# Optimization experiments

Measured on AMD Instinct MI355X. Metric: run time of the kernel, lower is better.

## Reference

```python
import jax, jax.numpy as jnp
import numpy as np
import math

N, T, C = 2, 2048, 2048   # batch, seq, dim_in
H, DQK, DV = 16, 128, 128  # heads, dim_qk, dim_v


def setup_inputs() -> dict:
    key = jax.random.key(0)
    ks = jax.random.split(key, 5)
    x = jax.random.normal(ks[0], (N, T, C), dtype=jnp.float32)
    # randw(*d) = randn(*d) / sqrt(d[-1]); last dim is dim_in=C for all weights
    scale = 1.0 / math.sqrt(C)
    w_q = jax.random.normal(ks[1], (H, DQK, C), dtype=jnp.float32) * scale
    w_k = jax.random.normal(ks[2], (H, DQK, C), dtype=jnp.float32) * scale
    w_v = jax.random.normal(ks[3], (H, DV, C), dtype=jnp.float32) * scale
    # original w_o is [DV*H, C]; stored here as its intended [H, DV, C] view
    w_o = jax.random.normal(ks[4], (H, DV, C), dtype=jnp.float32) * scale
    return {"x": x, "w_q": w_q, "w_k": w_k, "w_v": w_v, "w_o": w_o}


def reference(x, w_q, w_k, w_v, w_o):
    # QKV projections: [N,T,C] x [H,D,C] -> [N,H,T,D]
    q = jnp.einsum('ntc,hdc->nhtd', x, w_q)
    k = jnp.einsum('ntc,hdc->nhtd', x, w_k)
    v = jnp.einsum('ntc,hdc->nhtd', x, w_v)
    # attention scores [N,H,T,S]
    a = jnp.einsum('nhtd,nhsd->nhts', q, k) / math.sqrt(DQK)
    t = x.shape[1]
    causal_mask = jnp.tril(jnp.ones((t, t), dtype=bool))  # [T,S]
    a = jnp.where(causal_mask[None, None, :, :], a, -jnp.inf)
    a = jax.nn.softmax(a, axis=3)
    # dropout=0.0 -> no-op
    y = jnp.einsum('nhts,nhsd->nthd', a, v)  # [N,T,H,DV]
    out = jnp.einsum('nthd,hdc->ntc', y, w_o)
    return (out, k, v)
```

## Files before the change

### kernel.cpp

```cpp
#include <hip/hip_runtime.h>
#include <math.h>

#define NB 2
#define TT 2048
#define CC 2048
#define HH 16
#define DD 128

#define ELEMS_OUT ((size_t)NB * TT * CC)
#define ELEMS_KV  ((size_t)NB * HH * TT * DD)

typedef __attribute__((ext_vector_type(8))) short bf16x8;
typedef __attribute__((ext_vector_type(4))) float f32x4;

__device__ __forceinline__ void split_bf16(float v, unsigned short& hi, unsigned short& lo) {
    const unsigned u = __float_as_uint(v);
    hi = (unsigned short)(u >> 16);
    const float r = v - __uint_as_float(u & 0xffff0000u);
    lo = (unsigned short)(__float_as_uint(r) >> 16);
}

__device__ __forceinline__ unsigned short bf16_rtn(float v) {
    unsigned u = __float_as_uint(v);
    u += 0x7fff + ((u >> 16) & 1);
    return (unsigned short)(u >> 16);
}

__global__ __launch_bounds__(256)
void conv_hl(const float* __restrict__ src, unsigned short* __restrict__ hi,
             unsigned short* __restrict__ lo, int n4)
{
    for (int i = blockIdx.x * 256 + threadIdx.x; i < n4; i += gridDim.x * 256) {
        const float4 v = ((const float4*)src)[i];
        unsigned short h0, h1, h2, h3, l0, l1, l2, l3;
        split_bf16(v.x, h0, l0);
        split_bf16(v.y, h1, l1);
        split_bf16(v.z, h2, l2);
        split_bf16(v.w, h3, l3);
        ((ushort4*)hi)[i] = make_ushort4(h0, h1, h2, h3);
        ((ushort4*)lo)[i] = make_ushort4(l0, l1, l2, l3);
    }
}

__global__ __launch_bounds__(256)
void tconv_kernel(const float* __restrict__ src, unsigned short* __restrict__ dhi,
                  unsigned short* __restrict__ dlo)
{
    __shared__ float T[32][33];
    const int tx = threadIdx.x & 31;
    const int ty = threadIdx.x >> 5;
    const int c0 = blockIdx.x * 32;
    const int r0 = blockIdx.y * 32;
#pragma unroll
    for (int i = 0; i < 4; ++i)
        T[ty + 8 * i][tx] = src[(size_t)(r0 + ty + 8 * i) * 2048 + c0 + tx];
    __syncthreads();
#pragma unroll
    for (int i = 0; i < 4; ++i) {
        const float v = T[tx][ty + 8 * i];
        unsigned short h, l;
        split_bf16(v, h, l);
        const size_t o = (size_t)(c0 + ty + 8 * i) * 2048 + r0 + tx;
        dhi[o] = h;
        dlo[o] = l;
    }
}

#define MFMA_GEMM_BODY(AHI, ALO, BHI, BLO, M0, J0)                                   \
    const int tid  = threadIdx.x;                                                    \
    const int lane = tid & 63;                                                       \
    const int w    = tid >> 6;                                                       \
    const int wr   = w >> 1, wc = w & 1;                                             \
    const int lr   = lane & 15, g = lane >> 4;                                       \
    __shared__ __align__(16) unsigned short As[2][4][129][8];                        \
    __shared__ __align__(16) unsigned short Bs[2][4][129][8];                        \
    f32x4 acc[4][4];                                                                 \
    _Pragma("unroll")                                                                \
    for (int m = 0; m < 4; ++m)                                                      \
        _Pragma("unroll")                                                            \
        for (int n = 0; n < 4; ++n) acc[m][n] = (f32x4){0.f, 0.f, 0.f, 0.f};         \
    for (int kt = 0; kt < CC; kt += 32) {                                            \
        __syncthreads();                                                             \
        _Pragma("unroll")                                                            \
        for (int it = 0; it < 4; ++it) {                                             \
            const int hl   = it >> 1;                                                \
            const int rem  = tid + (it & 1) * 256;                                   \
            const int row  = rem >> 2;                                               \
            const int slot = rem & 3;                                                \
            const unsigned short* ap = (hl ? ALO : AHI)                              \
                + (size_t)(M0 + row) * 2048 + kt + slot * 8;                         \
            *(bf16x8*)&As[hl][slot][row][0] = *(const bf16x8*)ap;                    \
            const unsigned short* bp = (hl ? BLO : BHI)                              \
                + (size_t)(J0 + row) * 2048 + kt + slot * 8;                         \
            *(bf16x8*)&Bs[hl][slot][row][0] = *(const bf16x8*)bp;                    \
        }                                                                            \
        __syncthreads();                                                             \
        bf16x8 ah[4], al[4];                                                         \
        _Pragma("unroll")                                                            \
        for (int m = 0; m < 4; ++m) {                                                \
            ah[m] = *(const bf16x8*)&As[0][g][wr * 64 + m * 16 + lr][0];             \
            al[m] = *(const bf16x8*)&As[1][g][wr * 64 + m * 16 + lr][0];             \
        }                                                                            \
        _Pragma("unroll")                                                            \
        for (int n = 0; n < 4; ++n) {                                                \
            const bf16x8 bh = *(const bf16x8*)&Bs[0][g][wc * 64 + n * 16 + lr][0];   \
            const bf16x8 bl = *(const bf16x8*)&Bs[1][g][wc * 64 + n * 16 + lr][0];   \
            _Pragma("unroll")                                                        \
            for (int m = 0; m < 4; ++m) {                                            \
                f32x4 t = acc[m][n];                                                 \
                t = __builtin_amdgcn_mfma_f32_16x16x32_bf16(al[m], bh, t, 0, 0, 0);  \
                t = __builtin_amdgcn_mfma_f32_16x16x32_bf16(ah[m], bl, t, 0, 0, 0);  \
                t = __builtin_amdgcn_mfma_f32_16x16x32_bf16(ah[m], bh, t, 0, 0, 0);  \
                acc[m][n] = t;                                                       \
            }                                                                        \
        }                                                                            \
    }

__global__ __launch_bounds__(256, 3)
void mfma_qkv_kernel(const unsigned short* __restrict__ ahi,
                     const unsigned short* __restrict__ alo,
                     const unsigned short* __restrict__ bhi,
                     const unsigned short* __restrict__ blo,
                     float* __restrict__ qb, float* __restrict__ kb,
                     float* __restrict__ vb)
{
    const int j0 = blockIdx.x * 128;
    const int m0 = blockIdx.y * 128;
    MFMA_GEMM_BODY(ahi, alo, bhi, blo, m0, j0)

    const int p = j0 >> 11;
    const int h = (j0 & 2047) >> 7;
    float* outb = (p == 0) ? qb : ((p == 1) ? kb : vb);
#pragma unroll
    for (int m = 0; m < 4; ++m) {
#pragma unroll
        for (int r = 0; r < 4; ++r) {
            const int gm = m0 + wr * 64 + m * 16 + g * 4 + r;
            const int nb = gm >> 11;
            const int t  = gm & 2047;
            float* rowp = outb + ((size_t)(nb * HH + h) * TT + t) * DD;
#pragma unroll
            for (int n = 0; n < 4; ++n)
                rowp[wc * 64 + n * 16 + lr] = acc[m][n][r];
        }
    }
}

__global__ __launch_bounds__(256, 3)
void mfma_oproj_kernel(const unsigned short* __restrict__ ahi,
                       const unsigned short* __restrict__ alo,
                       const unsigned short* __restrict__ bhi,
                       const unsigned short* __restrict__ blo,
                       float* __restrict__ outp)
{
    const int j0 = blockIdx.x * 128;
    const int m0 = blockIdx.y * 128;
    MFMA_GEMM_BODY(ahi, alo, bhi, blo, m0, j0)

#pragma unroll
    for (int m = 0; m < 4; ++m) {
#pragma unroll
        for (int r = 0; r < 4; ++r) {
            const int gm = m0 + wr * 64 + m * 16 + g * 4 + r;
            float* rowp = outp + (size_t)gm * 2048 + j0;
#pragma unroll
            for (int n = 0; n < 4; ++n)
                rowp[wc * 64 + n * 16 + lr] = acc[m][n][r];
        }
    }
}

#define QBLK 128
#define KVB 64

__global__ __launch_bounds__(512, 1)
void attn_mfma_kernel(const float* __restrict__ qg,
                      const float* __restrict__ kg,
                      const float* __restrict__ vg,
                      unsigned short* __restrict__ yhi,
                      unsigned short* __restrict__ ylo)
{
    const int tid  = threadIdx.x;
    const int lane = tid & 63;
    const int w    = tid >> 6;
    const int lr   = lane & 15;
    const int g    = lane >> 4;
    const int bx   = blockIdx.x;
    const int qt   = 15 - (bx >> 5);
    const int nh   = bx & 31;
    const int n    = nh >> 4;
    const int h    = nh & 15;
    const int qr0  = qt * QBLK;

    const float* Q = qg + (size_t)nh * TT * DD;
    const float* K = kg + (size_t)nh * TT * DD;
    const float* V = vg + (size_t)nh * TT * DD;

    __shared__ __align__(16) unsigned short Ks[2][4][4][66][8];
    __shared__ __align__(16) unsigned short Vt[128][72];
    __shared__ __align__(16) unsigned short Ps[8][16][72];

    bf16x8 qh[4], ql[4];
    {
        const int qr = qr0 + w * 16 + lr;
#pragma unroll
        for (int kc = 0; kc < 4; ++kc) {
            const float* p = Q + (size_t)qr * DD + kc * 32 + g * 8;
            const float4 f0 = *(const float4*)p;
            const float4 f1 = *(const float4*)(p + 4);
            const float f[8] = {f0.x, f0.y, f0.z, f0.w, f1.x, f1.y, f1.z, f1.w};
            bf16x8 hv, lv;
#pragma unroll
            for (int j = 0; j < 8; ++j) {
                unsigned short hu, lu;
                split_bf16(f[j], hu, lu);
                hv[j] = (short)hu;
                lv[j] = (short)lu;
            }
            qh[kc] = hv;
            ql[kc] = lv;
        }
    }

    f32x4 o[8];
#pragma unroll
    for (int n2 = 0; n2 < 8; ++n2) o[n2] = (f32x4){0.f, 0.f, 0.f, 0.f};
    float m2[4], lsum[4];
#pragma unroll
    for (int r = 0; r < 4; ++r) { m2[r] = -INFINITY; lsum[r] = 0.f; }

    const float c2 = 0.08838834764831845f * 1.44269504088896f;

    const int jmax = 2 * qt + 1;
    for (int jt = 0; jt <= jmax; ++jt) {
        const int s0 = jt * KVB;

        __syncthreads();
#pragma unroll
        for (int it = 0; it < 2; ++it) {
            const int u  = tid + it * 512;
            const int s  = u >> 4;
            const int k8 = u & 15;
            const int kc = k8 >> 2, gg = k8 & 3;
            const float* p = K + (size_t)(s0 + s) * DD + k8 * 8;
            const float4 f0 = *(const float4*)p;
            const float4 f1 = *(const float4*)(p + 4);
            const float f[8] = {f0.x, f0.y, f0.z, f0.w, f1.x, f1.y, f1.z, f1.w};
            bf16x8 hv, lv;
#pragma unroll
            for (int j = 0; j < 8; ++j) {
                unsigned short hu, lu;
                split_bf16(f[j], hu, lu);
                hv[j] = (short)hu;
                lv[j] = (short)lu;
            }
            *(bf16x8*)&Ks[0][kc][gg][s][0] = hv;
            *(bf16x8*)&Ks[1][kc][gg][s][0] = lv;
        }
#pragma unroll
        for (int it = 0; it < 4; ++it) {
            const int u  = tid + it * 512;
            const int d4 = u & 31;
            const int s  = u >> 5;
            const float4 f = *(const float4*)(V + (size_t)(s0 + s) * DD + d4 * 4);
            Vt[d4 * 4 + 0][s] = bf16_rtn(f.x);
            Vt[d4 * 4 + 1][s] = bf16_rtn(f.y);
            Vt[d4 * 4 + 2][s] = bf16_rtn(f.z);
            Vt[d4 * 4 + 3][s] = bf16_rtn(f.w);
        }
        __syncthreads();

        f32x4 sa[4];
#pragma unroll
        for (int nn = 0; nn < 4; ++nn) {
            f32x4 t = (f32x4){0.f, 0.f, 0.f, 0.f};
#pragma unroll
            for (int kc = 0; kc < 4; ++kc) {
                const bf16x8 kh = *(const bf16x8*)&Ks[0][kc][g][nn * 16 + lr][0];
                const bf16x8 kl = *(const bf16x8*)&Ks[1][kc][g][nn * 16 + lr][0];
                t = __builtin_amdgcn_mfma_f32_16x16x32_bf16(ql[kc], kh, t, 0, 0, 0);
                t = __builtin_amdgcn_mfma_f32_16x16x32_bf16(qh[kc], kl, t, 0, 0, 0);
                t = __builtin_amdgcn_mfma_f32_16x16x32_bf16(qh[kc], kh, t, 0, 0, 0);
            }
            sa[nn] = t;
        }

        const int qbase = qr0 + w * 16 + g * 4;
        const bool domask = (s0 + 63 > qr0 + w * 16);
#pragma unroll
        for (int r = 0; r < 4; ++r) {
            float sv[4];
#pragma unroll
            for (int nn = 0; nn < 4; ++nn) {
                float s = sa[nn][r] * c2;
                if (domask && (s0 + nn * 16 + lr > qbase + r)) s = -INFINITY;
                sv[nn] = s;
            }
            float mr = fmaxf(fmaxf(sv[0], sv[1]), fmaxf(sv[2], sv[3]));
            mr = fmaxf(mr, __shfl_xor(mr, 1));
            mr = fmaxf(mr, __shfl_xor(mr, 2));
            mr = fmaxf(mr, __shfl_xor(mr, 4));
            mr = fmaxf(mr, __shfl_xor(mr, 8));
            const float mnew = fmaxf(m2[r], mr);
            const float corr = exp2f(m2[r] - mnew);
            m2[r] = mnew;
            float rs = 0.f;
#pragma unroll
            for (int nn = 0; nn < 4; ++nn) {
                const float pv = exp2f(sv[nn] - mnew);
                rs += pv;
                Ps[w][g * 4 + r][nn * 16 + lr] = bf16_rtn(pv);
            }
            rs += __shfl_xor(rs, 1);
            rs += __shfl_xor(rs, 2);
            rs += __shfl_xor(rs, 4);
            rs += __shfl_xor(rs, 8);
            lsum[r] = lsum[r] * corr + rs;
#pragma unroll
            for (int n2 = 0; n2 < 8; ++n2) o[n2][r] *= corr;
        }

#pragma unroll
        for (int kc2 = 0; kc2 < 2; ++kc2) {
            const bf16x8 pa = *(const bf16x8*)&Ps[w][lr][kc2 * 32 + g * 8];
#pragma unroll
            for (int n2 = 0; n2 < 8; ++n2) {
                const bf16x8 vb = *(const bf16x8*)&Vt[n2 * 16 + lr][kc2 * 32 + g * 8];
                o[n2] = __builtin_amdgcn_mfma_f32_16x16x32_bf16(pa, vb, o[n2], 0, 0, 0);
            }
        }
    }

#pragma unroll
    for (int r = 0; r < 4; ++r) {
        const float inv = 1.f / lsum[r];
        const int gm = n * 2048 + qr0 + w * 16 + g * 4 + r;
        const size_t base = (size_t)gm * 2048 + h * 128;
#pragma unroll
        for (int n2 = 0; n2 < 8; ++n2) {
            unsigned short hu, lu;
            split_bf16(o[n2][r] * inv, hu, lu);
            yhi[base + n2 * 16 + lr] = hu;
            ylo[base + n2 * 16 + lr] = lu;
        }
    }
}

__global__ __launch_bounds__(256, 1)
void attn_kernel(const float* __restrict__ qg,
                 const float* __restrict__ kg,
                 const float* __restrict__ vg,
                 float* __restrict__ yf32)
{
    const int tid = threadIdx.x;
    const int tx  = tid & 15;
    const int ty  = tid >> 4;
    const int qt  = blockIdx.x;
    const int nh  = blockIdx.y;
    const int n   = nh >> 4;
    const int h   = nh & 15;

    const float* Q = qg + (size_t)nh * TT * DD;
    const float* K = kg + (size_t)nh * TT * DD;
    const float* V = vg + (size_t)nh * TT * DD;

    __shared__ float Qs[64][128];
    __shared__ float Ks2[64][128];
    __shared__ float Vs[64][128];
    __shared__ float Ps2[64][68];

    const int qr0 = qt * 64;

#pragma unroll
    for (int it = 0; it < 8; ++it) {
        const int f4 = tid + it * 256;
        const int r  = f4 >> 5;
        const int c4 = f4 & 31;
        const float4 qv = *(const float4*)(Q + (size_t)(qr0 + r) * DD + c4 * 4);
        *(float4*)&Qs[r][(c4 ^ (r & 7)) << 2] = qv;
    }

    float acc[4][8];
#pragma unroll
    for (int i = 0; i < 4; ++i)
#pragma unroll
        for (int c = 0; c < 8; ++c) acc[i][c] = 0.f;

    float mrow[4], lrow[4];
#pragma unroll
    for (int i = 0; i < 4; ++i) { mrow[i] = -INFINITY; lrow[i] = 0.f; }

    const float sm_scale = 0.08838834764831845f;

    for (int jt = 0; jt <= qt; ++jt) {
        const int s0 = jt * 64;
        __syncthreads();
#pragma unroll
        for (int it = 0; it < 8; ++it) {
            const int f4 = tid + it * 256;
            const int r  = f4 >> 5;
            const int c4 = f4 & 31;
            const float4 kv = *(const float4*)(K + (size_t)(s0 + r) * DD + c4 * 4);
            *(float4*)&Ks2[r][(c4 ^ (r & 7)) << 2] = kv;
            const float4 vv = *(const float4*)(V + (size_t)(s0 + r) * DD + c4 * 4);
            *(float4*)&Vs[r][c4 << 2] = vv;
        }
        __syncthreads();

        float S[4][4];
#pragma unroll
        for (int i = 0; i < 4; ++i)
#pragma unroll
            for (int j = 0; j < 4; ++j) S[i][j] = 0.f;

#pragma unroll 8
        for (int k4 = 0; k4 < 32; ++k4) {
            const int bsl = (k4 ^ (tx & 7)) << 2;
            const float4 b0 = *(const float4*)&Ks2[tx     ][bsl];
            const float4 b1 = *(const float4*)&Ks2[tx + 16][bsl];
            const float4 b2 = *(const float4*)&Ks2[tx + 32][bsl];
            const float4 b3 = *(const float4*)&Ks2[tx + 48][bsl];
#pragma unroll
            for (int i = 0; i < 4; ++i) {
                const int r = ty * 4 + i;
                const float4 a = *(const float4*)&Qs[r][(k4 ^ (r & 7)) << 2];
                S[i][0] = fmaf(a.w, b0.w, fmaf(a.z, b0.z, fmaf(a.y, b0.y, fmaf(a.x, b0.x, S[i][0]))));
                S[i][1] = fmaf(a.w, b1.w, fmaf(a.z, b1.z, fmaf(a.y, b1.y, fmaf(a.x, b1.x, S[i][1]))));
                S[i][2] = fmaf(a.w, b2.w, fmaf(a.z, b2.z, fmaf(a.y, b2.y, fmaf(a.x, b2.x, S[i][2]))));
                S[i][3] = fmaf(a.w, b3.w, fmaf(a.z, b3.z, fmaf(a.y, b3.y, fmaf(a.x, b3.x, S[i][3]))));
            }
        }

        const bool diag = (jt == qt);
#pragma unroll
        for (int i = 0; i < 4; ++i)
#pragma unroll
            for (int j = 0; j < 4; ++j) {
                float s = S[i][j] * sm_scale;
                if (diag && (tx + 16 * j > ty * 4 + i)) s = -INFINITY;
                S[i][j] = s;
            }

#pragma unroll
        for (int i = 0; i < 4; ++i) {
            float tm = fmaxf(fmaxf(S[i][0], S[i][1]), fmaxf(S[i][2], S[i][3]));
            tm = fmaxf(tm, __shfl_xor(tm, 1, 16));
            tm = fmaxf(tm, __shfl_xor(tm, 2, 16));
            tm = fmaxf(tm, __shfl_xor(tm, 4, 16));
            tm = fmaxf(tm, __shfl_xor(tm, 8, 16));
            const float mnew = fmaxf(mrow[i], tm);
            const float corr = expf(mrow[i] - mnew);
            mrow[i] = mnew;
            float rs = 0.f;
#pragma unroll
            for (int j = 0; j < 4; ++j) {
                const float pv = expf(S[i][j] - mnew);
                S[i][j] = pv;
                rs += pv;
            }
            rs += __shfl_xor(rs, 1, 16);
            rs += __shfl_xor(rs, 2, 16);
            rs += __shfl_xor(rs, 4, 16);
            rs += __shfl_xor(rs, 8, 16);
            lrow[i] = lrow[i] * corr + rs;
#pragma unroll
            for (int c = 0; c < 8; ++c) acc[i][c] *= corr;
            const int r = ty * 4 + i;
#pragma unroll
            for (int j = 0; j < 4; ++j) Ps2[r][tx + 16 * j] = S[i][j];
        }
        __syncthreads();

#pragma unroll 4
        for (int s4 = 0; s4 < 16; ++s4) {
            const float4 p0 = *(const float4*)&Ps2[ty * 4 + 0][s4 * 4];
            const float4 p1 = *(const float4*)&Ps2[ty * 4 + 1][s4 * 4];
            const float4 p2 = *(const float4*)&Ps2[ty * 4 + 2][s4 * 4];
            const float4 p3 = *(const float4*)&Ps2[ty * 4 + 3][s4 * 4];
            const float pa[4][4] = {{p0.x, p0.y, p0.z, p0.w},
                                    {p1.x, p1.y, p1.z, p1.w},
                                    {p2.x, p2.y, p2.z, p2.w},
                                    {p3.x, p3.y, p3.z, p3.w}};
#pragma unroll
            for (int ww = 0; ww < 4; ++ww) {
                const int s = s4 * 4 + ww;
                const float4 va = *(const float4*)&Vs[s][tx * 4];
                const float4 vb = *(const float4*)&Vs[s][64 + tx * 4];
#pragma unroll
                for (int i = 0; i < 4; ++i) {
                    const float pv = pa[i][ww];
                    acc[i][0] = fmaf(pv, va.x, acc[i][0]);
                    acc[i][1] = fmaf(pv, va.y, acc[i][1]);
                    acc[i][2] = fmaf(pv, va.z, acc[i][2]);
                    acc[i][3] = fmaf(pv, va.w, acc[i][3]);
                    acc[i][4] = fmaf(pv, vb.x, acc[i][4]);
                    acc[i][5] = fmaf(pv, vb.y, acc[i][5]);
                    acc[i][6] = fmaf(pv, vb.z, acc[i][6]);
                    acc[i][7] = fmaf(pv, vb.w, acc[i][7]);
                }
            }
        }
    }

#pragma unroll
    for (int i = 0; i < 4; ++i) {
        const float inv = 1.f / lrow[i];
        const int qr = qr0 + ty * 4 + i;
        float* rowp = yf32 + (size_t)(n * 2048 + qr) * 2048 + h * 128;
        const float4 o0 = make_float4(acc[i][0] * inv, acc[i][1] * inv, acc[i][2] * inv, acc[i][3] * inv);
        const float4 o1 = make_float4(acc[i][4] * inv, acc[i][5] * inv, acc[i][6] * inv, acc[i][7] * inv);
        *(float4*)(rowp + tx * 4)      = o0;
        *(float4*)(rowp + 64 + tx * 4) = o1;
    }
}

__global__ __launch_bounds__(256, 2)
void qkv_proj_kernel(const float* __restrict__ x,
                     const float* __restrict__ wq,
                     const float* __restrict__ wk,
                     const float* __restrict__ wv,
                     float* __restrict__ q_buf,
                     float* __restrict__ k_out,
                     float* __restrict__ v_out)
{
    const int tid = threadIdx.x;
    const int tx  = tid & 15;
    const int ty  = tid >> 4;
    const int j0  = blockIdx.x * 128;
    const int m0  = blockIdx.y * 128;

    const int    p   = j0 >> 11;
    const int    jw0 = j0 & 2047;
    const float* W    = (p == 0) ? wq    : ((p == 1) ? wk    : wv);
    float*       outb = (p == 0) ? q_buf : ((p == 1) ? k_out : v_out);

    __shared__ float At[16][132];
    __shared__ float Bt[16][132];

    float acc[8][8];
#pragma unroll
    for (int i = 0; i < 8; ++i)
#pragma unroll
        for (int j = 0; j < 8; ++j) acc[i][j] = 0.f;

    for (int kt = 0; kt < CC; kt += 16) {
        __syncthreads();
#pragma unroll
        for (int it = 0; it < 2; ++it) {
            const int f4  = tid + it * 256;
            const int row = f4 >> 2;
            const int kf4 = f4 & 3;
            const float4 a = *(const float4*)(x + (size_t)(m0 + row) * CC + kt + kf4 * 4);
            At[kf4 * 4 + 0][row] = a.x;
            At[kf4 * 4 + 1][row] = a.y;
            At[kf4 * 4 + 2][row] = a.z;
            At[kf4 * 4 + 3][row] = a.w;
            const float4 b = *(const float4*)(W + (size_t)(jw0 + row) * CC + kt + kf4 * 4);
            Bt[kf4 * 4 + 0][row] = b.x;
            Bt[kf4 * 4 + 1][row] = b.y;
            Bt[kf4 * 4 + 2][row] = b.z;
            Bt[kf4 * 4 + 3][row] = b.w;
        }
        __syncthreads();

#pragma unroll
        for (int k = 0; k < 16; ++k) {
            const float4 a0 = *(const float4*)&At[k][ty * 4];
            const float4 a1 = *(const float4*)&At[k][64 + ty * 4];
            const float4 b0 = *(const float4*)&Bt[k][tx * 4];
            const float4 b1 = *(const float4*)&Bt[k][64 + tx * 4];
            const float av[8] = {a0.x, a0.y, a0.z, a0.w, a1.x, a1.y, a1.z, a1.w};
            const float bv[8] = {b0.x, b0.y, b0.z, b0.w, b1.x, b1.y, b1.z, b1.w};
#pragma unroll
            for (int i = 0; i < 8; ++i)
#pragma unroll
                for (int j = 0; j < 8; ++j)
                    acc[i][j] = fmaf(av[i], bv[j], acc[i][j]);
        }
    }

    const int h = jw0 >> 7;
#pragma unroll
    for (int rh = 0; rh < 2; ++rh) {
#pragma unroll
        for (int i = 0; i < 4; ++i) {
            const int m = m0 + rh * 64 + ty * 4 + i;
            const int n = m >> 11;
            const int t = m & 2047;
            float* rowp = outb + ((size_t)(n * HH + h) * TT + t) * DD;
            const int ai = rh * 4 + i;
            const float4 o0 = make_float4(acc[ai][0], acc[ai][1], acc[ai][2], acc[ai][3]);
            const float4 o1 = make_float4(acc[ai][4], acc[ai][5], acc[ai][6], acc[ai][7]);
            *(float4*)(rowp + tx * 4)      = o0;
            *(float4*)(rowp + 64 + tx * 4) = o1;
        }
    }
}

__global__ __launch_bounds__(256, 2)
void out_proj_kernel(const float* __restrict__ y,
                     const float* __restrict__ wo,
                     float* __restrict__ out)
{
    const int tid = threadIdx.x;
    const int tx  = tid & 15;
    const int ty  = tid >> 4;
    const int c0  = blockIdx.x * 128;
    const int m0  = blockIdx.y * 128;

    __shared__ float At[16][132];
    __shared__ float Bs2[16][132];

    float acc[8][8];
#pragma unroll
    for (int i = 0; i < 8; ++i)
#pragma unroll
        for (int j = 0; j < 8; ++j) acc[i][j] = 0.f;

    for (int kt = 0; kt < 2048; kt += 16) {
        __syncthreads();
#pragma unroll
        for (int it = 0; it < 2; ++it) {
            const int f4 = tid + it * 256;
            {
                const int row = f4 >> 2;
                const int kf4 = f4 & 3;
                const float4 a = *(const float4*)(y + (size_t)(m0 + row) * 2048 + kt + kf4 * 4);
                At[kf4 * 4 + 0][row] = a.x;
                At[kf4 * 4 + 1][row] = a.y;
                At[kf4 * 4 + 2][row] = a.z;
                At[kf4 * 4 + 3][row] = a.w;
            }
            {
                const int row = f4 >> 5;
                const int cf4 = f4 & 31;
                const float4 b = *(const float4*)(wo + (size_t)(kt + row) * 2048 + c0 + cf4 * 4);
                *(float4*)&Bs2[row][cf4 * 4] = b;
            }
        }
        __syncthreads();

#pragma unroll
        for (int k = 0; k < 16; ++k) {
            const float4 a0 = *(const float4*)&At[k][ty * 4];
            const float4 a1 = *(const float4*)&At[k][64 + ty * 4];
            const float4 b0 = *(const float4*)&Bs2[k][tx * 4];
            const float4 b1 = *(const float4*)&Bs2[k][64 + tx * 4];
            const float av[8] = {a0.x, a0.y, a0.z, a0.w, a1.x, a1.y, a1.z, a1.w};
            const float bv[8] = {b0.x, b0.y, b0.z, b0.w, b1.x, b1.y, b1.z, b1.w};
#pragma unroll
            for (int i = 0; i < 8; ++i)
#pragma unroll
                for (int j = 0; j < 8; ++j)
                    acc[i][j] = fmaf(av[i], bv[j], acc[i][j]);
        }
    }

#pragma unroll
    for (int rh = 0; rh < 2; ++rh) {
#pragma unroll
        for (int i = 0; i < 4; ++i) {
            const int m  = m0 + rh * 64 + ty * 4 + i;
            const int ai = rh * 4 + i;
#pragma unroll
            for (int ch = 0; ch < 2; ++ch) {
                const float4 o = make_float4(acc[ai][ch * 4 + 0], acc[ai][ch * 4 + 1],
                                             acc[ai][ch * 4 + 2], acc[ai][ch * 4 + 3]);
                *(float4*)(out + (size_t)m * 2048 + c0 + ch * 64 + tx * 4) = o;
            }
        }
    }
}

extern "C" void kernel_launch(void* const* d_in, const int* in_sizes, int n_in,
                              void* d_out, int out_size, void* d_ws, size_t ws_size,
                              hipStream_t stream)
{
    const float* x  = (const float*)d_in[0];
    const float* wq = (const float*)d_in[1];
    const float* wk = (const float*)d_in[2];
    const float* wv = (const float*)d_in[3];
    const float* wo = (const float*)d_in[4];

    float* out   = (float*)d_out;
    float* k_out = out + ELEMS_OUT;
    float* v_out = k_out + ELEMS_KV;
    float* q_buf = out;

    const size_t NEED = 134217728;
    if (ws_size >= NEED) {
        unsigned short* xhi   = (unsigned short*)d_ws;
        unsigned short* xlo   = xhi + 8388608;
        unsigned short* whi   = xlo + 8388608;
        unsigned short* wlo   = whi + 12582912;
        unsigned short* wothi = wlo + 12582912;
        unsigned short* wotlo = wothi + 4194304;
        unsigned short* yhi   = wotlo + 4194304;
        unsigned short* ylo   = yhi + 8388608;

        conv_hl<<<dim3(2048), dim3(256), 0, stream>>>(x, xhi, xlo, 2097152);
        conv_hl<<<dim3(1024), dim3(256), 0, stream>>>(wq, whi,           wlo,           1048576);
        conv_hl<<<dim3(1024), dim3(256), 0, stream>>>(wk, whi + 4194304, wlo + 4194304, 1048576);
        conv_hl<<<dim3(1024), dim3(256), 0, stream>>>(wv, whi + 8388608, wlo + 8388608, 1048576);
        tconv_kernel<<<dim3(64, 64), dim3(256), 0, stream>>>(wo, wothi, wotlo);

        mfma_qkv_kernel<<<dim3(48, 32), dim3(256), 0, stream>>>(xhi, xlo, whi, wlo,
                                                                q_buf, k_out, v_out);
        attn_mfma_kernel<<<dim3(512), dim3(512), 0, stream>>>(q_buf, k_out, v_out, yhi, ylo);
        mfma_oproj_kernel<<<dim3(16, 32), dim3(256), 0, stream>>>(yhi, ylo, wothi, wotlo, out);
    } else {
        float* y_buf = (float*)d_ws;
        qkv_proj_kernel<<<dim3(48, 32), dim3(256), 0, stream>>>(x, wq, wk, wv,
                                                                q_buf, k_out, v_out);
        attn_kernel<<<dim3(32, 32), dim3(256), 0, stream>>>(q_buf, k_out, v_out, y_buf);
        out_proj_kernel<<<dim3(16, 32), dim3(256), 0, stream>>>(y_buf, wo, out);
    }
}
```

Baseline: 760.6 us.

## Use direct global-to-LDS loads, larger QKV tiles, and precomputed bf16 K/V for attention

Replaces register-staged shared-memory fills in both GEMMs with global_load_lds 16-byte transfers into XOR-swizzled LDS tiles. The QKV GEMM tile grows to 256x128 with occupancy hint 2. K is pre-split into hi/lo bf16 and V pre-transposed to bf16 by separate kernels, so attention no longer converts them per block. Attention now runs 256 threads, each warp handling 32 query rows, with a balanced causal query-tile ordering. This aims to cut redundant conversion work and load latency, at the cost of extra kernel launches, extra global traffic and more register pressure.

After: 750.7 us. About the same (-1.3%).

```diff
diff --git a/kernel.cpp b/kernel.cpp
--- a/kernel.cpp
+++ b/kernel.cpp
@@ -24,6 +24,12 @@
     unsigned u = __float_as_uint(v);
     u += 0x7fff + ((u >> 16) & 1);
     return (unsigned short)(u >> 16);
+}
+
+__device__ __forceinline__ void gload16(const void* gsrc, void* ldst) {
+    __builtin_amdgcn_global_load_lds(
+        (const __attribute__((address_space(1))) void*)gsrc,
+        (__attribute__((address_space(3))) void*)ldst, 16, 0, 0);
 }
 
 __global__ __launch_bounds__(256)
@@ -66,57 +72,37 @@
     }
 }
 
-#define MFMA_GEMM_BODY(AHI, ALO, BHI, BLO, M0, J0)                                   \
-    const int tid  = threadIdx.x;                                                    \
-    const int lane = tid & 63;                                                       \
-    const int w    = tid >> 6;                                                       \
-    const int wr   = w >> 1, wc = w & 1;                                             \
-    const int lr   = lane & 15, g = lane >> 4;                                       \
-    __shared__ __align__(16) unsigned short As[2][4][129][8];                        \
-    __shared__ __align__(16) unsigned short Bs[2][4][129][8];                        \
-    f32x4 acc[4][4];                                                                 \
-    _Pragma("unroll")                                                                \
-    for (int m = 0; m < 4; ++m)                                                      \
-        _Pragma("unroll")                                                            \
-        for (int n = 0; n < 4; ++n) acc[m][n] = (f32x4){0.f, 0.f, 0.f, 0.f};         \
-    for (int kt = 0; kt < CC; kt += 32) {                                            \
-        __syncthreads();                                                             \
-        _Pragma("unroll")                                                            \
-        for (int it = 0; it < 4; ++it) {                                             \
-            const int hl   = it >> 1;                                                \
-            const int rem  = tid + (it & 1) * 256;                                   \
-            const int row  = rem >> 2;                                               \
-            const int slot = rem & 3;                                                \
-            const unsigned short* ap = (hl ? ALO : AHI)                              \
-                + (size_t)(M0 + row) * 2048 + kt + slot * 8;                         \
-            *(bf16x8*)&As[hl][slot][row][0] = *(const bf16x8*)ap;                    \
-            const unsigned short* bp = (hl ? BLO : BHI)                              \
-                + (size_t)(J0 + row) * 2048 + kt + slot * 8;                         \
-            *(bf16x8*)&Bs[hl][slot][row][0] = *(const bf16x8*)bp;                    \
-        }                                                                            \
-        __syncthreads();                                                             \
-        bf16x8 ah[4], al[4];                                                         \
-        _Pragma("unroll")                                                            \
-        for (int m = 0; m < 4; ++m) {                                                \
-            ah[m] = *(const bf16x8*)&As[0][g][wr * 64 + m * 16 + lr][0];             \
-            al[m] = *(const bf16x8*)&As[1][g][wr * 64 + m * 16 + lr][0];             \
-        }                                                                            \
-        _Pragma("unroll")                                                            \
-        for (int n = 0; n < 4; ++n) {                                                \
-            const bf16x8 bh = *(const bf16x8*)&Bs[0][g][wc * 64 + n * 16 + lr][0];   \
-            const bf16x8 bl = *(const bf16x8*)&Bs[1][g][wc * 64 + n * 16 + lr][0];   \
-            _Pragma("unroll")                                                        \
-            for (int m = 0; m < 4; ++m) {                                            \
-                f32x4 t = acc[m][n];                                                 \
-                t = __builtin_amdgcn_mfma_f32_16x16x32_bf16(al[m], bh, t, 0, 0, 0);  \
-                t = __builtin_amdgcn_mfma_f32_16x16x32_bf16(ah[m], bl, t, 0, 0, 0);  \
-                t = __builtin_amdgcn_mfma_f32_16x16x32_bf16(ah[m], bh, t, 0, 0, 0);  \
-                acc[m][n] = t;                                                       \
-            }                                                                        \
-        }                                                                            \
-    }
-
-__global__ __launch_bounds__(256, 3)
+__global__ __launch_bounds__(256)
+void vtrans_kernel(const float* __restrict__ v, unsigned short* __restrict__ vt)
+{
+    __shared__ __align__(16) unsigned short Td[128][72];
+    const int t  = threadIdx.x;
+    const int s0 = blockIdx.x * 64;
+    const int nh = blockIdx.y;
+    const float* src = v + (size_t)nh * TT * DD;
+#pragma unroll
+    for (int j = 0; j < 8; ++j) {
+        const int u  = t + j * 256;
+        const int s  = u >> 5;
+        const int d4 = u & 31;
+        const float4 f = *(const float4*)(src + (size_t)(s0 + s) * DD + d4 * 4);
+        Td[d4 * 4 + 0][s] = bf16_rtn(f.x);
+        Td[d4 * 4 + 1][s] = bf16_rtn(f.y);
+        Td[d4 * 4 + 2][s] = bf16_rtn(f.z);
+        Td[d4 * 4 + 3][s] = bf16_rtn(f.w);
+    }
+    __syncthreads();
+#pragma unroll
+    for (int j = 0; j < 4; ++j) {
+        const int u = t + j * 256;
+        const int d = u >> 3;
+        const int c = u & 7;
+        const bf16x8 val = *(const bf16x8*)&Td[d][c * 8];
+        *(bf16x8*)(vt + ((size_t)nh * DD + d) * TT + s0 + c * 8) = val;
+    }
+}
+
+__global__ __launch_bounds__(256, 2)
 void mfma_qkv_kernel(const unsigned short* __restrict__ ahi,
                      const unsigned short* __restrict__ alo,
                      const unsigned short* __restrict__ bhi,
@@ -124,24 +110,87 @@
                      float* __restrict__ qb, float* __restrict__ kb,
                      float* __restrict__ vb)
 {
-    const int j0 = blockIdx.x * 128;
-    const int m0 = blockIdx.y * 128;
-    MFMA_GEMM_BODY(ahi, alo, bhi, blo, m0, j0)
+    const int tid  = threadIdx.x;
+    const int lane = tid & 63;
+    const int w    = tid >> 6;
+    const int wr   = w >> 1, wc = w & 1;
+    const int lr   = lane & 15, g = lane >> 4;
+    const int j0   = blockIdx.x * 128;
+    const int m0   = blockIdx.y * 256;
+
+    __shared__ __align__(16) unsigned short As[2][256][32];
+    __shared__ __align__(16) unsigned short Bs[2][128][32];
+
+    f32x4 acc[8][4];
+#pragma unroll
+    for (int mi = 0; mi < 8; ++mi)
+#pragma unroll
+        for (int ni = 0; ni < 4; ++ni) acc[mi][ni] = (f32x4){0.f, 0.f, 0.f, 0.f};
+
+    const int crow = lane >> 2;
+    const int asl  = lane & 3;
+
+    for (int kt = 0; kt < CC; kt += 32) {
+        __syncthreads();
+#pragma unroll
+        for (int hl = 0; hl < 2; ++hl) {
+            const unsigned short* Ap = hl ? alo : ahi;
+            const unsigned short* Bp = hl ? blo : bhi;
+#pragma unroll
+            for (int i = 0; i < 4; ++i) {
+                const int row = (i * 4 + w) * 16 + crow;
+                const int sg  = asl ^ (row & 3);
+                gload16(Ap + (size_t)(m0 + row) * 2048 + kt + sg * 8,
+                        &As[hl][row][asl * 8]);
+            }
+#pragma unroll
+            for (int i = 0; i < 2; ++i) {
+                const int row = (i * 4 + w) * 16 + crow;
+                const int sg  = asl ^ (row & 3);
+                gload16(Bp + (size_t)(j0 + row) * 2048 + kt + sg * 8,
+                        &Bs[hl][row][asl * 8]);
+            }
+        }
+        __syncthreads();
+
+        bf16x8 ah[8], al[8];
+        const int sp = (g ^ (lr & 3)) * 8;
+#pragma unroll
+        for (int mi = 0; mi < 8; ++mi) {
+            const int row = wr * 128 + mi * 16 + lr;
+            ah[mi] = *(const bf16x8*)&As[0][row][sp];
+            al[mi] = *(const bf16x8*)&As[1][row][sp];
+        }
+#pragma unroll
+        for (int ni = 0; ni < 4; ++ni) {
+            const int row = wc * 64 + ni * 16 + lr;
+            const bf16x8 bh = *(const bf16x8*)&Bs[0][row][sp];
+            const bf16x8 bl = *(const bf16x8*)&Bs[1][row][sp];
+#pragma unroll
+            for (int mi = 0; mi < 8; ++mi) {
+                f32x4 t = acc[mi][ni];
+                t = __builtin_amdgcn_mfma_f32_16x16x32_bf16(al[mi], bh, t, 0, 0, 0);
+                t = __builtin_amdgcn_mfma_f32_16x16x32_bf16(ah[mi], bl, t, 0, 0, 0);
+                t = __builtin_amdgcn_mfma_f32_16x16x32_bf16(ah[mi], bh, t, 0, 0, 0);
+                acc[mi][ni] = t;
+            }
+        }
+    }
 
     const int p = j0 >> 11;
     const int h = (j0 & 2047) >> 7;
     float* outb = (p == 0) ? qb : ((p == 1) ? kb : vb);
 #pragma unroll
-    for (int m = 0; m < 4; ++m) {
+    for (int mi = 0; mi < 8; ++mi) {
 #pragma unroll
         for (int r = 0; r < 4; ++r) {
-            const int gm = m0 + wr * 64 + m * 16 + g * 4 + r;
+            const int gm = m0 + wr * 128 + mi * 16 + g * 4 + r;
             const int nb = gm >> 11;
             const int t  = gm & 2047;
             float* rowp = outb + ((size_t)(nb * HH + h) * TT + t) * DD;
 #pragma unroll
-            for (int n = 0; n < 4; ++n)
-                rowp[wc * 64 + n * 16 + lr] = acc[m][n][r];
+            for (int ni = 0; ni < 4; ++ni)
+                rowp[wc * 64 + ni * 16 + lr] = acc[mi][ni][r];
         }
     }
 }
@@ -153,30 +202,88 @@
                        const unsigned short* __restrict__ blo,
                        float* __restrict__ outp)
 {
-    const int j0 = blockIdx.x * 128;
-    const int m0 = blockIdx.y * 128;
-    MFMA_GEMM_BODY(ahi, alo, bhi, blo, m0, j0)
-
-#pragma unroll
-    for (int m = 0; m < 4; ++m) {
+    const int tid  = threadIdx.x;
+    const int lane = tid & 63;
+    const int w    = tid >> 6;
+    const int wr   = w >> 1, wc = w & 1;
+    const int lr   = lane & 15, g = lane >> 4;
+    const int j0   = blockIdx.x * 128;
+    const int m0   = blockIdx.y * 128;
+
+    __shared__ __align__(16) unsigned short As[2][128][32];
+    __shared__ __align__(16) unsigned short Bs[2][128][32];
+
+    f32x4 acc[4][4];
+#pragma unroll
+    for (int mi = 0; mi < 4; ++mi)
+#pragma unroll
+        for (int ni = 0; ni < 4; ++ni) acc[mi][ni] = (f32x4){0.f, 0.f, 0.f, 0.f};
+
+    const int crow = lane >> 2;
+    const int asl  = lane & 3;
+
+    for (int kt = 0; kt < CC; kt += 32) {
+        __syncthreads();
+#pragma unroll
+        for (int hl = 0; hl < 2; ++hl) {
+            const unsigned short* Ap = hl ? alo : ahi;
+            const unsigned short* Bp = hl ? blo : bhi;
+#pragma unroll
+            for (int i = 0; i < 2; ++i) {
+                const int row = (i * 4 + w) * 16 + crow;
+                const int sg  = asl ^ (row & 3);
+                gload16(Ap + (size_t)(m0 + row) * 2048 + kt + sg * 8,
+                        &As[hl][row][asl * 8]);
+                gload16(Bp + (size_t)(j0 + row) * 2048 + kt + sg * 8,
+                        &Bs[hl][row][asl * 8]);
+            }
+        }
+        __syncthreads();
+
+        bf16x8 ah[4], al[4];
+        const int sp = (g ^ (lr & 3)) * 8;
+#pragma unroll
+        for (int mi = 0; mi < 4; ++mi) {
+            const int row = wr * 64 + mi * 16 + lr;
+            ah[mi] = *(const bf16x8*)&As[0][row][sp];
+            al[mi] = *(const bf16x8*)&As[1][row][sp];
+        }
+#pragma unroll
+        for (int ni = 0; ni < 4; ++ni) {
+            const int row = wc * 64 + ni * 16 + lr;
+            const bf16x8 bh = *(const bf16x8*)&Bs[0][row][sp];
+            const bf16x8 bl = *(const bf16x8*)&Bs[1][row][sp];
+#pragma unroll
+            for (int mi = 0; mi < 4; ++mi) {
+                f32x4 t = acc[mi][ni];
+                t = __builtin_amdgcn_mfma_f32_16x16x32_bf16(al[mi], bh, t, 0, 0, 0);
+                t = __builtin_amdgcn_mfma_f32_16x16x32_bf16(ah[mi], bl, t, 0, 0, 0);
+                t = __builtin_amdgcn_mfma_f32_16x16x32_bf16(ah[mi], bh, t, 0, 0, 0);
+                acc[mi][ni] = t;
+            }
+        }
+    }
+
+#pragma unroll
+    for (int mi = 0; mi < 4; ++mi) {
 #pragma unroll
         for (int r = 0; r < 4; ++r) {
-            const int gm = m0 + wr * 64 + m * 16 + g * 4 + r;
+            const int gm = m0 + wr * 64 + mi * 16 + g * 4 + r;
             float* rowp = outp + (size_t)gm * 2048 + j0;
 #pragma unroll
-            for (int n = 0; n < 4; ++n)
-                rowp[wc * 64 + n * 16 + lr] = acc[m][n][r];
-        }
-    }
-}
-
-#define QBLK 128
+            for (int ni = 0; ni < 4; ++ni)
+                rowp[wc * 64 + ni * 16 + lr] = acc[mi][ni][r];
+        }
+    }
+}
+
 #define KVB 64
 
-__global__ __launch_bounds__(512, 1)
+__global__ __launch_bounds__(256, 2)
 void attn_mfma_kernel(const float* __restrict__ qg,
-                      const float* __restrict__ kg,
-                      const float* __restrict__ vg,
+                      const unsigned short* __restrict__ khi,
+                      const unsigned short* __restrict__ klo,
+                      const unsigned short* __restrict__ vtg,
                       unsigned short* __restrict__ yhi,
                       unsigned short* __restrict__ ylo)
 {
@@ -186,23 +293,26 @@
     const int lr   = lane & 15;
     const int g    = lane >> 4;
     const int bx   = blockIdx.x;
-    const int qt   = 15 - (bx >> 5);
+    const int g2   = bx >> 5;
     const int nh   = bx & 31;
+    const int qt   = (g2 < 8) ? (15 - g2) : (g2 - 8);
     const int n    = nh >> 4;
     const int h    = nh & 15;
-    const int qr0  = qt * QBLK;
-
-    const float* Q = qg + (size_t)nh * TT * DD;
-    const float* K = kg + (size_t)nh * TT * DD;
-    const float* V = vg + (size_t)nh * TT * DD;
-
-    __shared__ __align__(16) unsigned short Ks[2][4][4][66][8];
-    __shared__ __align__(16) unsigned short Vt[128][72];
-    __shared__ __align__(16) unsigned short Ps[8][16][72];
-
-    bf16x8 qh[4], ql[4];
-    {
-        const int qr = qr0 + w * 16 + lr;
+    const int qr0  = qt * 128;
+
+    const float*          Q  = qg  + (size_t)nh * TT * DD;
+    const unsigned short* Kh = khi + (size_t)nh * TT * DD;
+    const unsigned short* Kl = klo + (size_t)nh * TT * DD;
+    const unsigned short* Vt = vtg + (size_t)nh * DD * TT;
+
+    __shared__ __align__(16) unsigned short Ks[2][64][128];
+    __shared__ __align__(16) unsigned short Vs[128][64];
+    __shared__ __align__(16) unsigned short Ps[4][32][72];
+
+    bf16x8 qh[2][4], ql[2][4];
+#pragma unroll
+    for (int mf = 0; mf < 2; ++mf) {
+        const int qr = qr0 + w * 32 + mf * 16 + lr;
 #pragma unroll
         for (int kc = 0; kc < 4; ++kc) {
             const float* p = Q + (size_t)qr * DD + kc * 32 + g * 8;
@@ -217,17 +327,21 @@
                 hv[j] = (short)hu;
                 lv[j] = (short)lu;
             }
-            qh[kc] = hv;
-            ql[kc] = lv;
-        }
-    }
-
-    f32x4 o[8];
-#pragma unroll
-    for (int n2 = 0; n2 < 8; ++n2) o[n2] = (f32x4){0.f, 0.f, 0.f, 0.f};
-    float m2[4], lsum[4];
-#pragma unroll
-    for (int r = 0; r < 4; ++r) { m2[r] = -INFINITY; lsum[r] = 0.f; }
+            qh[mf][kc] = hv;
+            ql[mf][kc] = lv;
+        }
+    }
+
+    f32x4 o[2][8];
+#pragma unroll
+    for (int mf = 0; mf < 2; ++mf)
+#pragma unroll
+        for (int n2 = 0; n2 < 8; ++n2) o[mf][n2] = (f32x4){0.f, 0.f, 0.f, 0.f};
+    float m2[2][4], ls[2][4];
+#pragma unroll
+    for (int mf = 0; mf < 2; ++mf)
+#pragma unroll
+        for (int r = 0; r < 4; ++r) { m2[mf][r] = -INFINITY; ls[mf][r] = 0.f; }
 
     const float c2 = 0.08838834764831845f * 1.44269504088896f;
 
@@ -237,111 +351,115 @@
 
         __syncthreads();
 #pragma unroll
-        for (int it = 0; it < 2; ++it) {
-            const int u  = tid + it * 512;
-            const int s  = u >> 4;
-            const int k8 = u & 15;
-            const int kc = k8 >> 2, gg = k8 & 3;
-            const float* p = K + (size_t)(s0 + s) * DD + k8 * 8;
-            const float4 f0 = *(const float4*)p;
-            const float4 f1 = *(const float4*)(p + 4);
-            const float f[8] = {f0.x, f0.y, f0.z, f0.w, f1.x, f1.y, f1.z, f1.w};
-            bf16x8 hv, lv;
-#pragma unroll
-            for (int j = 0; j < 8; ++j) {
+        for (int i = 0; i < 8; ++i) {
+            const int chunk = i * 4 + w;
+            const int hl = chunk >> 4;
+            const int cl = chunk & 15;
+            const int sl = cl * 4 + (lane >> 4);
+            const int sp2 = lane & 15;
+            const int sg  = sp2 ^ (sl & 7);
+            gload16((hl ? Kl : Kh) + (size_t)(s0 + sl) * 128 + sg * 8,
+                    &Ks[hl][sl][sp2 * 8]);
+        }
+#pragma unroll
+        for (int i = 0; i < 4; ++i) {
+            const int chunk = i * 4 + w;
+            const int dl  = chunk * 8 + (lane >> 3);
+            const int sp2 = lane & 7;
+            const int sg  = sp2 ^ (dl & 7);
+            gload16(Vt + (size_t)dl * TT + s0 + sg * 8, &Vs[dl][sp2 * 8]);
+        }
+        __syncthreads();
+
+        f32x4 sa[2][4];
+#pragma unroll
+        for (int mf = 0; mf < 2; ++mf)
+#pragma unroll
+            for (int nn = 0; nn < 4; ++nn) sa[mf][nn] = (f32x4){0.f, 0.f, 0.f, 0.f};
+#pragma unroll
+        for (int nn = 0; nn < 4; ++nn) {
+#pragma unroll
+            for (int kc = 0; kc < 4; ++kc) {
+                const int sp2 = ((kc * 4 + g) ^ (lr & 7)) * 8;
+                const bf16x8 kh = *(const bf16x8*)&Ks[0][nn * 16 + lr][sp2];
+                const bf16x8 kl = *(const bf16x8*)&Ks[1][nn * 16 + lr][sp2];
+#pragma unroll
+                for (int mf = 0; mf < 2; ++mf) {
+                    f32x4 t = sa[mf][nn];
+                    t = __builtin_amdgcn_mfma_f32_16x16x32_bf16(ql[mf][kc], kh, t, 0, 0, 0);
+                    t = __builtin_amdgcn_mfma_f32_16x16x32_bf16(qh[mf][kc], kl, t, 0, 0, 0);
+                    t = __builtin_amdgcn_mfma_f32_16x16x32_bf16(qh[mf][kc], kh, t, 0, 0, 0);
+                    sa[mf][nn] = t;
+                }
+            }
+        }
+
+#pragma unroll
+        for (int mf = 0; mf < 2; ++mf) {
+            const int  qbase  = qr0 + w * 32 + mf * 16 + g * 4;
+            const bool domask = (s0 + 63 > qr0 + w * 32 + mf * 16);
+#pragma unroll
+            for (int r = 0; r < 4; ++r) {
+                float sv[4];
+#pragma unroll
+                for (int nn = 0; nn < 4; ++nn) {
+                    float s = sa[mf][nn][r] * c2;
+                    if (domask && (s0 + nn * 16 + lr > qbase + r)) s = -INFINITY;
+                    sv[nn] = s;
+                }
+                float mr = fmaxf(fmaxf(sv[0], sv[1]), fmaxf(sv[2], sv[3]));
+                mr = fmaxf(mr, __shfl_xor(mr, 1));
+                mr = fmaxf(mr, __shfl_xor(mr, 2));
+                mr = fmaxf(mr, __shfl_xor(mr, 4));
+                mr = fmaxf(mr, __shfl_xor(mr, 8));
+                const float mnew = fmaxf(m2[mf][r], mr);
+                const float corr = exp2f(m2[mf][r] - mnew);
+                m2[mf][r] = mnew;
+                float rs = 0.f;
+#pragma unroll
+                for (int nn = 0; nn < 4; ++nn) {
+                    const float pv = exp2f(sv[nn] - mnew);
+                    rs += pv;
+                    Ps[w][mf * 16 + g * 4 + r][nn * 16 + lr] = bf16_rtn(pv);
+                }
+                rs += __shfl_xor(rs, 1);
+                rs += __shfl_xor(rs, 2);
+                rs += __shfl_xor(rs, 4);
+                rs += __shfl_xor(rs, 8);
+                ls[mf][r] = ls[mf][r] * corr + rs;
+#pragma unroll
+                for (int n2 = 0; n2 < 8; ++n2) o[mf][n2][r] *= corr;
+            }
+        }
+
+#pragma unroll
+        for (int kc2 = 0; kc2 < 2; ++kc2) {
+            const bf16x8 pa0 = *(const bf16x8*)&Ps[w][lr][kc2 * 32 + g * 8];
+            const bf16x8 pa1 = *(const bf16x8*)&Ps[w][16 + lr][kc2 * 32 + g * 8];
+#pragma unroll
+            for (int n2 = 0; n2 < 8; ++n2) {
+                const int sp2 = ((kc2 * 4 + g) ^ (lr & 7)) * 8;
+                const bf16x8 vb = *(const bf16x8*)&Vs[n2 * 16 + lr][sp2];
+                o[0][n2] = __builtin_amdgcn_mfma_f32_16x16x32_bf16(pa0, vb, o[0][n2], 0, 0, 0);
+                o[1][n2] = __builtin_amdgcn_mfma_f32_16x16x32_bf16(pa1, vb, o[1][n2], 0, 0, 0);
+            }
+        }
+    }
+
+#pragma unroll
+    for (int mf = 0; mf < 2; ++mf) {
+#pragma unroll
+        for (int r = 0; r < 4; ++r) {
+            const float inv = 1.f / ls[mf][r];
+            const int gm = n * 2048 + qr0 + w * 32 + mf * 16 + g * 4 + r;
+            const size_t base = (size_t)gm * 2048 + h * 128;
+#pragma unroll
+            for (int n2 = 0; n2 < 8; ++n2) {
                 unsigned short hu, lu;
-                split_bf16(f[j], hu, lu);
-                hv[j] = (short)hu;
-                lv[j] = (short)lu;
-            }
-            *(bf16x8*)&Ks[0][kc][gg][s][0] = hv;
-            *(bf16x8*)&Ks[1][kc][gg][s][0] = lv;
-        }
-#pragma unroll
-        for (int it = 0; it < 4; ++it) {
-            const int u  = tid + it * 512;
-            const int d4 = u & 31;
-            const int s  = u >> 5;
-            const float4 f = *(const float4*)(V + (size_t)(s0 + s) * DD + d4 * 4);
-            Vt[d4 * 4 + 0][s] = bf16_rtn(f.x);
-            Vt[d4 * 4 + 1][s] = bf16_rtn(f.y);
-            Vt[d4 * 4 + 2][s] = bf16_rtn(f.z);
-            Vt[d4 * 4 + 3][s] = bf16_rtn(f.w);
-        }
-        __syncthreads();
-
-        f32x4 sa[4];
-#pragma unroll
-        for (int nn = 0; nn < 4; ++nn) {
-            f32x4 t = (f32x4){0.f, 0.f, 0.f, 0.f};
-#pragma unroll
-            for (int kc = 0; kc < 4; ++kc) {
-                const bf16x8 kh = *(const bf16x8*)&Ks[0][kc][g][nn * 16 + lr][0];
-                const bf16x8 kl = *(const bf16x8*)&Ks[1][kc][g][nn * 16 + lr][0];
-                t = __builtin_amdgcn_mfma_f32_16x16x32_bf16(ql[kc], kh, t, 0, 0, 0);
-                t = __builtin_amdgcn_mfma_f32_16x16x32_bf16(qh[kc], kl, t, 0, 0, 0);
-                t = __builtin_amdgcn_mfma_f32_16x16x32_bf16(qh[kc], kh, t, 0, 0, 0);
-            }
-            sa[nn] = t;
-        }
-
-        const int qbase = qr0 + w * 16 + g * 4;
-        const bool domask = (s0 + 63 > qr0 + w * 16);
-#pragma unroll
-        for (int r = 0; r < 4; ++r) {
-            float sv[4];
-#pragma unroll
-            for (int nn = 0; nn < 4; ++nn) {
-                float s = sa[nn][r] * c2;
-                if (domask && (s0 + nn * 16 + lr > qbase + r)) s = -INFINITY;
-                sv[nn] = s;
-            }
-            float mr = fmaxf(fmaxf(sv[0], sv[1]), fmaxf(sv[2], sv[3]));
-            mr = fmaxf(mr, __shfl_xor(mr, 1));
-            mr = fmaxf(mr, __shfl_xor(mr, 2));
-            mr = fmaxf(mr, __shfl_xor(mr, 4));
-            mr = fmaxf(mr, __shfl_xor(mr, 8));
-            const float mnew = fmaxf(m2[r], mr);
-            const float corr = exp2f(m2[r] - mnew);
-            m2[r] = mnew;
-            float rs = 0.f;
-#pragma unroll
-            for (int nn = 0; nn < 4; ++nn) {
-                const float pv = exp2f(sv[nn] - mnew);
-                rs += pv;
-                Ps[w][g * 4 + r][nn * 16 + lr] = bf16_rtn(pv);
-            }
-            rs += __shfl_xor(rs, 1);
-            rs += __shfl_xor(rs, 2);
-            rs += __shfl_xor(rs, 4);
-            rs += __shfl_xor(rs, 8);
-            lsum[r] = lsum[r] * corr + rs;
-#pragma unroll
-            for (int n2 = 0; n2 < 8; ++n2) o[n2][r] *= corr;
-        }
-
-#pragma unroll
-        for (int kc2 = 0; kc2 < 2; ++kc2) {
-            const bf16x8 pa = *(const bf16x8*)&Ps[w][lr][kc2 * 32 + g * 8];
-#pragma unroll
-            for (int n2 = 0; n2 < 8; ++n2) {
-                const bf16x8 vb = *(const bf16x8*)&Vt[n2 * 16 + lr][kc2 * 32 + g * 8];
-                o[n2] = __builtin_amdgcn_mfma_f32_16x16x32_bf16(pa, vb, o[n2], 0, 0, 0);
-            }
-        }
-    }
-
-#pragma unroll
-    for (int r = 0; r < 4; ++r) {
-        const float inv = 1.f / lsum[r];
-        const int gm = n * 2048 + qr0 + w * 16 + g * 4 + r;
-        const size_t base = (size_t)gm * 2048 + h * 128;
-#pragma unroll
-        for (int n2 = 0; n2 < 8; ++n2) {
-            unsigned short hu, lu;
-            split_bf16(o[n2][r] * inv, hu, lu);
-            yhi[base + n2 * 16 + lr] = hu;
-            ylo[base + n2 * 16 + lr] = lu;
+                split_bf16(o[mf][n2][r] * inv, hu, lu);
+                yhi[base + n2 * 16 + lr] = hu;
+                ylo[base + n2 * 16 + lr] = lu;
+            }
         }
     }
 }
@@ -366,7 +484,7 @@
 
     __shared__ float Qs[64][128];
     __shared__ float Ks2[64][128];
-    __shared__ float Vs[64][128];
+    __shared__ float Vs2[64][128];
     __shared__ float Ps2[64][68];
 
     const int qr0 = qt * 64;
@@ -403,7 +521,7 @@
             const float4 kv = *(const float4*)(K + (size_t)(s0 + r) * DD + c4 * 4);
             *(float4*)&Ks2[r][(c4 ^ (r & 7)) << 2] = kv;
             const float4 vv = *(const float4*)(V + (size_t)(s0 + r) * DD + c4 * 4);
-            *(float4*)&Vs[r][c4 << 2] = vv;
+            *(float4*)&Vs2[r][c4 << 2] = vv;
         }
         __syncthreads();
 
@@ -484,8 +602,8 @@
 #pragma unroll
             for (int ww = 0; ww < 4; ++ww) {
                 const int s = s4 * 4 + ww;
-                const float4 va = *(const float4*)&Vs[s][tx * 4];
-                const float4 vb = *(const float4*)&Vs[s][64 + tx * 4];
+                const float4 va = *(const float4*)&Vs2[s][tx * 4];
+                const float4 vb = *(const float4*)&Vs2[s][64 + tx * 4];
 #pragma unroll
                 for (int i = 0; i < 4; ++i) {
                     const float pv = pa[i][ww];
@@ -698,15 +816,24 @@
         unsigned short* yhi   = wotlo + 4194304;
         unsigned short* ylo   = yhi + 8388608;
 
+        unsigned short* khi = xhi;
+        unsigned short* klo = xlo;
+        unsigned short* vt  = whi;
+
         conv_hl<<<dim3(2048), dim3(256), 0, stream>>>(x, xhi, xlo, 2097152);
         conv_hl<<<dim3(1024), dim3(256), 0, stream>>>(wq, whi,           wlo,           1048576);
         conv_hl<<<dim3(1024), dim3(256), 0, stream>>>(wk, whi + 4194304, wlo + 4194304, 1048576);
         conv_hl<<<dim3(1024), dim3(256), 0, stream>>>(wv, whi + 8388608, wlo + 8388608, 1048576);
         tconv_kernel<<<dim3(64, 64), dim3(256), 0, stream>>>(wo, wothi, wotlo);
 
-        mfma_qkv_kernel<<<dim3(48, 32), dim3(256), 0, stream>>>(xhi, xlo, whi, wlo,
+        mfma_qkv_kernel<<<dim3(48, 16), dim3(256), 0, stream>>>(xhi, xlo, whi, wlo,
                                                                 q_buf, k_out, v_out);
-        attn_mfma_kernel<<<dim3(512), dim3(512), 0, stream>>>(q_buf, k_out, v_out, yhi, ylo);
+
+        conv_hl<<<dim3(2048), dim3(256), 0, stream>>>(k_out, khi, klo, 2097152);
+        vtrans_kernel<<<dim3(32, 32), dim3(256), 0, stream>>>(v_out, vt);
+
+        attn_mfma_kernel<<<dim3(512), dim3(256), 0, stream>>>(q_buf, khi, klo, vt,
+                                                              yhi, ylo);
         mfma_oproj_kernel<<<dim3(16, 32), dim3(256), 0, stream>>>(yhi, ylo, wothi, wotlo, out);
     } else {
         float* y_buf = (float*)d_ws;
```
